# Kernel tuning notes

Hardware: AMD Instinct MI355X
Metric: run time of the kernel (lower is better)

The kernel has to match this reference:

```python
import jax, jax.numpy as jnp
import numpy as np

N_EMBED = 8192
EMBED_DIM = 256


def setup_inputs() -> dict:
    key = jax.random.key(0)
    k1, k2 = jax.random.split(key)
    hidden_states = jax.random.normal(k1, (8, EMBED_DIM, 32, 32), dtype=jnp.float32)
    # original inits uniform(-1/n_e, 1/n_e); scale is irrelevant for correctness testing
    emb_weights = jax.random.uniform(
        k2, (N_EMBED, EMBED_DIM), dtype=jnp.float32,
        minval=-1.0 / N_EMBED, maxval=1.0 / N_EMBED)
    return {"hidden_states": hidden_states, "emb_weights": emb_weights}


def reference(hidden_states, emb_weights):
    # (B,C,H,W) -> (B,H,W,C)
    B, C, H, W = hidden_states.shape
    z = jnp.transpose(hidden_states, (0, 2, 3, 1))
    z_flat = z.reshape(-1, C)  # [B*H*W, C]
    # squared euclidean distance: ||z||^2 + ||e||^2 - 2 z e^T
    dist = (jnp.sum(z_flat ** 2, axis=1, keepdims=True)
            + jnp.sum(emb_weights ** 2, axis=1)
            - 2.0 * jnp.matmul(z_flat, emb_weights.T))  # [N, n_embed]
    min_encoding_indices = jnp.argmin(dist, axis=1)  # [N]
    z_q = emb_weights[min_encoding_indices].reshape(B, H, W, C)
    z_q = jnp.transpose(z_q, (0, 3, 1, 2))  # (B,C,H,W)
    min_encoding_indices = min_encoding_indices.reshape(B, -1)
    return z_q, min_encoding_indices
```

## Files before the change

### kernel.cpp

```cpp
#include <hip/hip_runtime.h>
#include <hip/hip_bf16.h>
#include <math.h>

#define C_DIM 256
#define N_EMB 8192
#define N_Z   8192
#define HWB   1024
#define MBLK  128
#define NSPLIT 4
#define SPLITC (N_EMB / NSPLIT)
#define NT    128
#define NTILES (SPLITC / NT)
#define NCHUNK (NTILES * 2)
#define CK    32
#define EPS   1.1e-3f
#define ZQ_ELEMS (N_Z * C_DIM)

typedef __attribute__((ext_vector_type(8))) short bf16x8;
typedef __attribute__((ext_vector_type(4))) float f32x4;
typedef unsigned short u16;
typedef unsigned int u32;

__device__ __forceinline__ float sqf(float x) { return __fmul_rn(x, x); }

__device__ __forceinline__ u16 f2bf(float v) {
  __hip_bfloat16 h = __float2bfloat16(v);
  u16 r; __builtin_memcpy(&r, &h, 2); return r;
}

__device__ __forceinline__ void g2l16(const u16* g, u16* l) {
  __builtin_amdgcn_global_load_lds(
      (const __attribute__((address_space(1))) unsigned int*)(const void*)g,
      (__attribute__((address_space(3))) unsigned int*)(void*)l, 16, 0, 0);
}

template <int STRIDE>
__device__ float pw_sumsq_256(const float* __restrict__ a) {
  float h[2];
#pragma unroll
  for (int hh = 0; hh < 2; ++hh) {
    const float* p = a + hh * 128 * STRIDE;
    float r0 = sqf(p[0 * STRIDE]), r1 = sqf(p[1 * STRIDE]);
    float r2 = sqf(p[2 * STRIDE]), r3 = sqf(p[3 * STRIDE]);
    float r4 = sqf(p[4 * STRIDE]), r5 = sqf(p[5 * STRIDE]);
    float r6 = sqf(p[6 * STRIDE]), r7 = sqf(p[7 * STRIDE]);
    for (int i = 8; i < 128; i += 8) {
      r0 = __fadd_rn(r0, sqf(p[(i + 0) * STRIDE]));
      r1 = __fadd_rn(r1, sqf(p[(i + 1) * STRIDE]));
      r2 = __fadd_rn(r2, sqf(p[(i + 2) * STRIDE]));
      r3 = __fadd_rn(r3, sqf(p[(i + 3) * STRIDE]));
      r4 = __fadd_rn(r4, sqf(p[(i + 4) * STRIDE]));
      r5 = __fadd_rn(r5, sqf(p[(i + 5) * STRIDE]));
      r6 = __fadd_rn(r6, sqf(p[(i + 6) * STRIDE]));
      r7 = __fadd_rn(r7, sqf(p[(i + 7) * STRIDE]));
    }
    h[hh] = __fadd_rn(__fadd_rn(__fadd_rn(r0, r1), __fadd_rn(r2, r3)),
                      __fadd_rn(__fadd_rn(r4, r5), __fadd_rn(r6, r7)));
  }
  return __fadd_rn(h[0], h[1]);
}

__device__ __forceinline__ float exact_score(const float* __restrict__ zr,
                                             const float* __restrict__ er,
                                             float z2v, float e2v) {
  float d = 0.f;
  for (int k4 = 0; k4 < 64; ++k4) {
    float4 a4 = *(const float4*)(zr + k4 * 4);
    float4 b4 = *(const float4*)(er + k4 * 4);
    d = fmaf(a4.x, b4.x, d); d = fmaf(a4.y, b4.y, d);
    d = fmaf(a4.z, b4.z, d); d = fmaf(a4.w, b4.w, d);
  }
  return __fsub_rn(__fadd_rn(z2v, e2v), __fmul_rn(2.f, d));
}

__global__ void vq_tr(const float* __restrict__ hid, float* __restrict__ zt,
                      u16* __restrict__ zbf) {
  __shared__ float tl[32][33];
  int t = threadIdx.x;
  int tx = t & 31, ty = t >> 5;
  int bb = blockIdx.x >> 8;
  int r = blockIdx.x & 255;
  int cT = r >> 5, hwT = r & 31;
#pragma unroll
  for (int p = 0; p < 4; ++p)
    tl[ty + p * 8][tx] =
        hid[((size_t)bb * C_DIM + cT * 32 + ty + p * 8) * HWB + hwT * 32 + tx];
  __syncthreads();
#pragma unroll
  for (int p = 0; p < 4; ++p) {
    float v = tl[tx][ty + p * 8];
    size_t oi = ((size_t)bb * HWB + hwT * 32 + ty + p * 8) * C_DIM + cT * 32 + tx;
    zt[oi] = v;
    zbf[oi] = f2bf(v);
  }
}

__global__ void vq_norms(const float* __restrict__ zt, const float* __restrict__ emb,
                         float* __restrict__ z2, float* __restrict__ e2,
                         u16* __restrict__ ebf) {
  int t = threadIdx.x, b = blockIdx.x;
  if (b < 32) {
    int r = b * 256 + t;
    e2[r] = pw_sumsq_256<1>(emb + (size_t)r * C_DIM);
    for (int k4 = 0; k4 < 64; ++k4) {
      float4 v = *(const float4*)(emb + (size_t)r * C_DIM + k4 * 4);
      ushort4 o;
      o.x = f2bf(v.x); o.y = f2bf(v.y); o.z = f2bf(v.z); o.w = f2bf(v.w);
      *(ushort4*)(ebf + (size_t)r * C_DIM + k4 * 4) = o;
    }
  } else {
    int n = (b - 32) * 256 + t;
    z2[n] = pw_sumsq_256<1>(zt + (size_t)n * C_DIM);
  }
}

__global__ __launch_bounds__(512, 2) void vq_filter(
    const u16* __restrict__ zbf, const u16* __restrict__ ebf,
    const float* __restrict__ zt, const float* __restrict__ emb,
    const float* __restrict__ z2g, const float* __restrict__ e2g,
    float* __restrict__ cd, int* __restrict__ ci) {
  __shared__ u16 el[2][16384];
  __shared__ u32 mrow[MBLK];
  __shared__ u16 rcol[MBLK * CK];
  __shared__ int rcnt[MBLK];
  __shared__ int ovfr[16];
  __shared__ int novf;
  __shared__ float wbs[8];
  __shared__ int wis[8];

  int t = threadIdx.x;
  int mb = blockIdx.x >> 2;
  int ns = blockIdx.x & 3;
  int n0z = mb * MBLK;
  int l = t & 63;
  int w = t >> 6;
  int wr = w >> 1, wc = w & 1;

  if (t < MBLK) { rcnt[t] = 0; mrow[t] = 0x7f800000u; }
  if (t == 0) novf = 0;

  bf16x8 A[2][8];
#pragma unroll
  for (int rf = 0; rf < 2; ++rf)
#pragma unroll
    for (int f = 0; f < 8; ++f)
      A[rf][f] = *(const bf16x8*)(zbf +
          (size_t)(n0z + wr * 32 + rf * 16 + (l & 15)) * C_DIM + f * 32 + ((l >> 4) << 3));

  float z2r[2][4];
#pragma unroll
  for (int rf = 0; rf < 2; ++rf)
#pragma unroll
    for (int r = 0; r < 4; ++r)
      z2r[rf][r] = z2g[n0z + wr * 32 + rf * 16 + (l >> 4) * 4 + r];

  float mpl[2][4];
#pragma unroll
  for (int rf = 0; rf < 2; ++rf)
#pragma unroll
    for (int r = 0; r < 4; ++r) mpl[rf][r] = INFINITY;

  const f32x4 vzero = {0.f, 0.f, 0.f, 0.f};
  const u16* esplit = ebf + (size_t)(ns * SPLITC) * C_DIM;

#define STAGE_E(nb_, c_)                                                      \
  {                                                                           \
    int tn_ = (c_) >> 1, kcn_ = ((c_) & 1) << 7;                              \
    const u16* bs_ = esplit + (size_t)(tn_ * NT) * C_DIM + kcn_;              \
    _Pragma("unroll")                                                         \
    for (int p_ = 0; p_ < 4; ++p_) {                                          \
      int o_ = (w * 4 + p_) * 64 + l;                                         \
      int g2_ = o_ >> 10, rr_ = (o_ >> 3) & 127, p3_ = o_ & 7;                \
      g2l16(bs_ + (size_t)rr_ * C_DIM + g2_ * 64 + ((p3_ ^ (rr_ & 7)) << 3),  \
            &el[nb_][(w * 4 + p_) * 512]);                                    \
    }                                                                         \
  }

  STAGE_E(0, 0)
  __syncthreads();

  int cur = 0;
#pragma unroll 1
  for (int pass = 0; pass < 2; ++pass) {
#pragma unroll 1
    for (int tile = 0; tile < NTILES; ++tile) {
      int ne0 = ns * SPLITC + tile * NT;
      f32x4 acc[2][4];
#pragma unroll
      for (int rf = 0; rf < 2; ++rf)
#pragma unroll
        for (int cf = 0; cf < 4; ++cf) acc[rf][cf] = vzero;

#pragma unroll
      for (int half = 0; half < 2; ++half) {
        int c = tile * 2 + half;
        if (!(pass == 1 && c == NCHUNK - 1)) STAGE_E(cur ^ 1, (c + 1) & (NCHUNK - 1))
#pragma unroll
        for (int kf = 0; kf < 4; ++kf) {
          int g2 = kf >> 1, ks = kf & 1;
          int phys = (((ks * 4 + (l >> 4)) ^ (l & 7)) << 3);
#pragma unroll
          for (int cf = 0; cf < 4; ++cf) {
            bf16x8 bfr = *(const bf16x8*)(&el[cur][g2 * 8192 +
                           (wc * 64 + cf * 16 + (l & 15)) * 64 + phys]);
            acc[0][cf] = __builtin_amdgcn_mfma_f32_16x16x32_bf16(A[0][half * 4 + kf], bfr, acc[0][cf], 0, 0, 0);
            acc[1][cf] = __builtin_amdgcn_mfma_f32_16x16x32_bf16(A[1][half * 4 + kf], bfr, acc[1][cf], 0, 0, 0);
          }
        }
        __syncthreads();
        cur ^= 1;
      }
      float e2s[4];
#pragma unroll
      for (int cf = 0; cf < 4; ++cf)
        e2s[cf] = e2g[ne0 + wc * 64 + cf * 16 + (l & 15)];
      if (pass == 0) {
#pragma unroll
        for (int rf = 0; rf < 2; ++rf)
#pragma unroll
          for (int r = 0; r < 4; ++r) {
            float z2v = z2r[rf][r];
            float mn = mpl[rf][r];
#pragma unroll
            for (int cf = 0; cf < 4; ++cf)
              mn = fminf(mn, fmaf(-2.f, acc[rf][cf][r], z2v + e2s[cf]));
            mpl[rf][r] = mn;
          }
      } else {
#pragma unroll
        for (int rf = 0; rf < 2; ++rf)
#pragma unroll
          for (int r = 0; r < 4; ++r) {
            int rowl = wr * 32 + rf * 16 + (l >> 4) * 4 + r;
            float z2v = z2r[rf][r];
            float thr = mpl[rf][r];
#pragma unroll
            for (int cf = 0; cf < 4; ++cf) {
              float s = fmaf(-2.f, acc[rf][cf][r], z2v + e2s[cf]);
              if (s <= thr) {
                int pos = atomicAdd(&rcnt[rowl], 1);
                if (pos < CK)
                  rcol[rowl * CK + pos] = (u16)(ne0 + wc * 64 + cf * 16 + (l & 15));
              }
            }
          }
      }
    }
    if (pass == 0) {
#pragma unroll
      for (int rf = 0; rf < 2; ++rf)
#pragma unroll
        for (int r = 0; r < 4; ++r) {
          float mn = mpl[rf][r];
#pragma unroll
          for (int m = 1; m < 16; m <<= 1)
            mn = fminf(mn, __shfl_xor(mn, m, 64));
          if ((l & 15) == 0) {
            int rowl = wr * 32 + rf * 16 + (l >> 4) * 4 + r;
            atomicMin(&mrow[rowl], __float_as_uint(mn));
          }
        }
      __syncthreads();
#pragma unroll
      for (int rf = 0; rf < 2; ++rf)
#pragma unroll
        for (int r = 0; r < 4; ++r) {
          int rowl = wr * 32 + rf * 16 + (l >> 4) * 4 + r;
          mpl[rf][r] = __uint_as_float(mrow[rowl]) + EPS;
        }
    }
  }
  __syncthreads();

  {
    int row = t >> 2;
    int cnt = rcnt[row];
    float b = INFINITY; int bi = N_EMB;
    if (cnt <= CK) {
      const float* zr = zt + (size_t)(n0z + row) * C_DIM;
      float z2v = z2g[n0z + row];
      for (int p2 = (t & 3); p2 < cnt; p2 += 4) {
        int col = rcol[row * CK + p2];
        float s = exact_score(zr, emb + (size_t)col * C_DIM, z2v, e2g[col]);
        if (s < b || (s == b && col < bi)) { b = s; bi = col; }
      }
    }
#pragma unroll
    for (int m = 1; m <= 2; m <<= 1) {
      float ob = __shfl_xor(b, m, 64);
      int oi2 = __shfl_xor(bi, m, 64);
      if (ob < b || (ob == b && oi2 < bi)) { b = ob; bi = oi2; }
    }
    if ((t & 3) == 0 && cnt <= CK) {
      cd[ns * N_Z + n0z + row] = b;
      ci[ns * N_Z + n0z + row] = bi;
    }
  }

  if (t < MBLK && rcnt[t] > CK) {
    int p = atomicAdd(&novf, 1);
    if (p < 16) ovfr[p] = t;
  }
  __syncthreads();
  int no = min(novf, 16);
  for (int oi = 0; oi < no; ++oi) {
    int row = ovfr[oi];
    const float* zr = zt + (size_t)(n0z + row) * C_DIM;
    float z2v = z2g[n0z + row];
    float b = INFINITY; int bi = N_EMB;
#pragma unroll
    for (int q = 0; q < 4; ++q) {
      int col = ns * SPLITC + t * 4 + q;
      float s = exact_score(zr, emb + (size_t)col * C_DIM, z2v, e2g[col]);
      if (s < b || (s == b && col < bi)) { b = s; bi = col; }
    }
#pragma unroll
    for (int m = 1; m <= 32; m <<= 1) {
      float ob = __shfl_xor(b, m, 64);
      int oi2 = __shfl_xor(bi, m, 64);
      if (ob < b || (ob == b && oi2 < bi)) { b = ob; bi = oi2; }
    }
    if (l == 0) { wbs[w] = b; wis[w] = bi; }
    __syncthreads();
    if (t == 0) {
      for (int w2 = 1; w2 < 8; ++w2)
        if (wbs[w2] < b || (wbs[w2] == b && wis[w2] < bi)) { b = wbs[w2]; bi = wis[w2]; }
      cd[ns * N_Z + n0z + row] = b;
      ci[ns * N_Z + n0z + row] = bi;
    }
    __syncthreads();
  }
}

__global__ void vq_out(const float* __restrict__ emb, const float* __restrict__ cd,
                       const int* __restrict__ ci, float* __restrict__ out) {
  __shared__ int sidx[32];
  int t = threadIdx.x;
  int n0 = blockIdx.x * 32;
  if (t < 32) {
    int n = n0 + t;
    float b = INFINITY;
    int bi = 0;
    for (int ns = 0; ns < NSPLIT; ++ns) {
      float d = cd[ns * N_Z + n];
      int i = ci[ns * N_Z + n];
      if (d < b || (d == b && i < bi)) { b = d; bi = i; }
    }
    sidx[t] = bi;
    out[ZQ_ELEMS + n] = (float)bi;
  }
  __syncthreads();
  int bb = n0 >> 10, hw0 = n0 & 1023;
  int nl = t & 31, cg = t >> 5;
#pragma unroll
  for (int p = 0; p < 8; ++p) {
    int c0 = cg * 4 + p * 32;
    float4 v = *(const float4*)(emb + (size_t)sidx[nl] * C_DIM + c0);
    out[((size_t)bb * C_DIM + c0 + 0) * HWB + hw0 + nl] = v.x;
    out[((size_t)bb * C_DIM + c0 + 1) * HWB + hw0 + nl] = v.y;
    out[((size_t)bb * C_DIM + c0 + 2) * HWB + hw0 + nl] = v.z;
    out[((size_t)bb * C_DIM + c0 + 3) * HWB + hw0 + nl] = v.w;
  }
}

extern "C" void kernel_launch(void* const* d_in, const int* in_sizes, int n_in,
                              void* d_out, int out_size, void* d_ws, size_t ws_size,
                              hipStream_t stream) {
  const float* hid = (const float*)d_in[0];
  const float* emb = (const float*)d_in[1];
  float* out = (float*)d_out;

  float* zt = (float*)d_ws;
  float* z2 = zt + (size_t)N_Z * C_DIM;
  float* e2 = z2 + N_Z;
  float* cd = e2 + N_EMB;
  int* ci = (int*)(cd + (size_t)NSPLIT * N_Z);
  u16* zbf = (u16*)(ci + (size_t)NSPLIT * N_Z);
  u16* ebf = zbf + (size_t)N_Z * C_DIM;

  vq_tr<<<2048, 256, 0, stream>>>(hid, zt, zbf);
  vq_norms<<<64, 256, 0, stream>>>(zt, emb, z2, e2, ebf);
  vq_filter<<<(N_Z / MBLK) * NSPLIT, 512, 0, stream>>>(zbf, ebf, zt, emb, z2, e2, cd, ci);
  vq_out<<<N_Z / 32, 256, 0, stream>>>(emb, cd, ci, out);
}
```

Measured before the change: 221.9 us.

## Retile VQ filter kernel: 256-row blocks, 8 codebook splits, 64-wide tiles

Changes the block tiling so each block owns 256 z rows (32 per wave) and an eighth of the codebook, with each tile holding 64 codebook entries. Every wave now covers all columns of a tile instead of splitting columns across two waves, so the LDS staging buffer shrinks by half and more A-fragment reuse happens per loaded B tile. The rescoring and overflow paths are adjusted to match: two threads per row, up to 32 overflow rows, and two columns per thread. In exchange there are twice as many split partial results to reduce, and more synchronisation per unit of MFMA work because the tiles are smaller.

```diff
diff --git a/kernel.cpp b/kernel.cpp
--- a/kernel.cpp
+++ b/kernel.cpp
@@ -6,10 +6,10 @@
 #define N_EMB 8192
 #define N_Z   8192
 #define HWB   1024
-#define MBLK  128
-#define NSPLIT 4
+#define MBLK  256
+#define NSPLIT 8
 #define SPLITC (N_EMB / NSPLIT)
-#define NT    128
+#define NT    64
 #define NTILES (SPLITC / NT)
 #define NCHUNK (NTILES * 2)
 #define CK    32
@@ -119,22 +119,22 @@
     const float* __restrict__ zt, const float* __restrict__ emb,
     const float* __restrict__ z2g, const float* __restrict__ e2g,
     float* __restrict__ cd, int* __restrict__ ci) {
-  __shared__ u16 el[2][16384];
+  __shared__ u16 el[2][8192];
   __shared__ u32 mrow[MBLK];
   __shared__ u16 rcol[MBLK * CK];
   __shared__ int rcnt[MBLK];
-  __shared__ int ovfr[16];
+  __shared__ int ovfr[32];
   __shared__ int novf;
   __shared__ float wbs[8];
   __shared__ int wis[8];
 
   int t = threadIdx.x;
-  int mb = blockIdx.x >> 2;
-  int ns = blockIdx.x & 3;
+  int mb = blockIdx.x >> 3;
+  int ns = blockIdx.x & 7;
   int n0z = mb * MBLK;
   int l = t & 63;
   int w = t >> 6;
-  int wr = w >> 1, wc = w & 1;
+  int x = l & 15, hi = l >> 4;
 
   if (t < MBLK) { rcnt[t] = 0; mrow[t] = 0x7f800000u; }
   if (t == 0) novf = 0;
@@ -145,14 +145,14 @@
 #pragma unroll
     for (int f = 0; f < 8; ++f)
       A[rf][f] = *(const bf16x8*)(zbf +
-          (size_t)(n0z + wr * 32 + rf * 16 + (l & 15)) * C_DIM + f * 32 + ((l >> 4) << 3));
+          (size_t)(n0z + w * 32 + rf * 16 + x) * C_DIM + f * 32 + hi * 8);
 
   float z2r[2][4];
 #pragma unroll
   for (int rf = 0; rf < 2; ++rf)
 #pragma unroll
     for (int r = 0; r < 4; ++r)
-      z2r[rf][r] = z2g[n0z + wr * 32 + rf * 16 + (l >> 4) * 4 + r];
+      z2r[rf][r] = z2g[n0z + w * 32 + rf * 16 + hi * 4 + r];
 
   float mpl[2][4];
 #pragma unroll
@@ -168,11 +168,11 @@
     int tn_ = (c_) >> 1, kcn_ = ((c_) & 1) << 7;                              \
     const u16* bs_ = esplit + (size_t)(tn_ * NT) * C_DIM + kcn_;              \
     _Pragma("unroll")                                                         \
-    for (int p_ = 0; p_ < 4; ++p_) {                                          \
-      int o_ = (w * 4 + p_) * 64 + l;                                         \
-      int g2_ = o_ >> 10, rr_ = (o_ >> 3) & 127, p3_ = o_ & 7;                \
+    for (int p_ = 0; p_ < 2; ++p_) {                                          \
+      int o_ = (w * 2 + p_) * 64 + l;                                         \
+      int g2_ = o_ >> 9, rr_ = (o_ >> 3) & 63, p3_ = o_ & 7;                  \
       g2l16(bs_ + (size_t)rr_ * C_DIM + g2_ * 64 + ((p3_ ^ (rr_ & 7)) << 3),  \
-            &el[nb_][(w * 4 + p_) * 512]);                                    \
+            &el[nb_][(w * 2 + p_) * 512]);                                    \
     }                                                                         \
   }
 
@@ -198,11 +198,11 @@
 #pragma unroll
         for (int kf = 0; kf < 4; ++kf) {
           int g2 = kf >> 1, ks = kf & 1;
-          int phys = (((ks * 4 + (l >> 4)) ^ (l & 7)) << 3);
+          int phys = (((ks * 4 + hi) ^ (l & 7)) << 3);
 #pragma unroll
           for (int cf = 0; cf < 4; ++cf) {
-            bf16x8 bfr = *(const bf16x8*)(&el[cur][g2 * 8192 +
-                           (wc * 64 + cf * 16 + (l & 15)) * 64 + phys]);
+            bf16x8 bfr = *(const bf16x8*)(&el[cur][g2 * 4096 +
+                           (cf * 16 + x) * 64 + phys]);
             acc[0][cf] = __builtin_amdgcn_mfma_f32_16x16x32_bf16(A[0][half * 4 + kf], bfr, acc[0][cf], 0, 0, 0);
             acc[1][cf] = __builtin_amdgcn_mfma_f32_16x16x32_bf16(A[1][half * 4 + kf], bfr, acc[1][cf], 0, 0, 0);
           }
@@ -213,7 +213,7 @@
       float e2s[4];
 #pragma unroll
       for (int cf = 0; cf < 4; ++cf)
-        e2s[cf] = e2g[ne0 + wc * 64 + cf * 16 + (l & 15)];
+        e2s[cf] = e2g[ne0 + cf * 16 + x];
       if (pass == 0) {
 #pragma unroll
         for (int rf = 0; rf < 2; ++rf)
@@ -231,7 +231,7 @@
         for (int rf = 0; rf < 2; ++rf)
 #pragma unroll
           for (int r = 0; r < 4; ++r) {
-            int rowl = wr * 32 + rf * 16 + (l >> 4) * 4 + r;
+            int rowl = w * 32 + rf * 16 + hi * 4 + r;
             float z2v = z2r[rf][r];
             float thr = mpl[rf][r];
 #pragma unroll
@@ -240,7 +240,7 @@
               if (s <= thr) {
                 int pos = atomicAdd(&rcnt[rowl], 1);
                 if (pos < CK)
-                  rcol[rowl * CK + pos] = (u16)(ne0 + wc * 64 + cf * 16 + (l & 15));
+                  rcol[rowl * CK + pos] = (u16)(ne0 + cf * 16 + x);
               }
             }
           }
@@ -253,10 +253,10 @@
         for (int r = 0; r < 4; ++r) {
           float mn = mpl[rf][r];
 #pragma unroll
-          for (int m = 1; m < 16; m <<= 1)
+          for (int m = 1; m <= 8; m <<= 1)
             mn = fminf(mn, __shfl_xor(mn, m, 64));
-          if ((l & 15) == 0) {
-            int rowl = wr * 32 + rf * 16 + (l >> 4) * 4 + r;
+          if (x == 0) {
+            int rowl = w * 32 + rf * 16 + hi * 4 + r;
             atomicMin(&mrow[rowl], __float_as_uint(mn));
           }
         }
@@ -265,7 +265,7 @@
       for (int rf = 0; rf < 2; ++rf)
 #pragma unroll
         for (int r = 0; r < 4; ++r) {
-          int rowl = wr * 32 + rf * 16 + (l >> 4) * 4 + r;
+          int rowl = w * 32 + rf * 16 + hi * 4 + r;
           mpl[rf][r] = __uint_as_float(mrow[rowl]) + EPS;
         }
     }
@@ -273,44 +273,41 @@
   __syncthreads();
 
   {
-    int row = t >> 2;
+    int row = t >> 1;
     int cnt = rcnt[row];
     float b = INFINITY; int bi = N_EMB;
     if (cnt <= CK) {
       const float* zr = zt + (size_t)(n0z + row) * C_DIM;
       float z2v = z2g[n0z + row];
-      for (int p2 = (t & 3); p2 < cnt; p2 += 4) {
+      for (int p2 = (t & 1); p2 < cnt; p2 += 2) {
         int col = rcol[row * CK + p2];
         float s = exact_score(zr, emb + (size_t)col * C_DIM, z2v, e2g[col]);
         if (s < b || (s == b && col < bi)) { b = s; bi = col; }
       }
-    }
-#pragma unroll
-    for (int m = 1; m <= 2; m <<= 1) {
-      float ob = __shfl_xor(b, m, 64);
-      int oi2 = __shfl_xor(bi, m, 64);
+      float ob = __shfl_xor(b, 1, 64);
+      int oi2 = __shfl_xor(bi, 1, 64);
       if (ob < b || (ob == b && oi2 < bi)) { b = ob; bi = oi2; }
-    }
-    if ((t & 3) == 0 && cnt <= CK) {
-      cd[ns * N_Z + n0z + row] = b;
-      ci[ns * N_Z + n0z + row] = bi;
+      if ((t & 1) == 0) {
+        cd[ns * N_Z + n0z + row] = b;
+        ci[ns * N_Z + n0z + row] = bi;
+      }
     }
   }
 
   if (t < MBLK && rcnt[t] > CK) {
     int p = atomicAdd(&novf, 1);
-    if (p < 16) ovfr[p] = t;
-  }
-  __syncthreads();
-  int no = min(novf, 16);
+    if (p < 32) ovfr[p] = t;
+  }
+  __syncthreads();
+  int no = min(novf, 32);
   for (int oi = 0; oi < no; ++oi) {
     int row = ovfr[oi];
     const float* zr = zt + (size_t)(n0z + row) * C_DIM;
     float z2v = z2g[n0z + row];
     float b = INFINITY; int bi = N_EMB;
 #pragma unroll
-    for (int q = 0; q < 4; ++q) {
-      int col = ns * SPLITC + t * 4 + q;
+    for (int q = 0; q < 2; ++q) {
+      int col = ns * SPLITC + t * 2 + q;
       float s = exact_score(zr, emb + (size_t)col * C_DIM, z2v, e2g[col]);
       if (s < b || (s == b && col < bi)) { b = s; bi = col; }
     }
```

Result: slower. 252.9 us (+14.0%).
